# Kernel tuning notes

Hardware: AMD Instinct MI355X
Metric: run time of the kernel (lower is better)

The kernel has to match this reference:

```python
import jax, jax.numpy as jnp
import numpy as np

B, DIN, H, DOUT = 8192, 1024, 2048, 1024
P, E = 4, 6            # n_patches, n_edges
C = H // P             # per-patch feature dim = 512
IDX_I = jnp.array([0, 0, 0, 1, 1, 2])  # i<j pair order matches nested loop
IDX_J = jnp.array([1, 2, 3, 2, 3, 3])


def setup_inputs() -> dict:
    key = jax.random.key(0)
    ks = jax.random.split(key, 12)
    s = 0.02
    return {
        "x": jax.random.normal(ks[0], (B, DIN), jnp.float32),
        "fiber": jax.random.normal(ks[1], (B, C), jnp.float32),  # randn_like(base) in torch fwd
        "W_in": jax.random.normal(ks[2], (DIN, H), jnp.float32) * s,
        "b_in": jnp.zeros((H,), jnp.float32),
        "incidence": jax.random.normal(ks[3], (E, P), jnp.float32) * 0.1,
        "sheaf_maps": jnp.tile((jnp.eye(C, dtype=jnp.float32) * 0.1)[None], (E, 1, 1)),
        "damping": jnp.float32(0.1),
        "Wb": jax.random.normal(ks[4], (P, C, C // 2), jnp.float32) * s,
        "bb": jnp.zeros((P, C // 2), jnp.float32),
        "Wf": jax.random.normal(ks[5], (P, C, C // 2), jnp.float32) * s,
        "bf": jnp.zeros((P, C // 2), jnp.float32),
        "Wt": jax.random.normal(ks[6], (C, C), jnp.float32) * s,
        "bt": jnp.zeros((C,), jnp.float32),
        "Wr": jax.random.normal(ks[7], (E, C, C // 2), jnp.float32) * s,
        "br": jnp.zeros((E, C // 2), jnp.float32),
        "Wg": jax.random.normal(ks[8], (H, H), jnp.float32) * s,
        "bg": jnp.zeros((H,), jnp.float32),
        "Wc": jax.random.normal(ks[9], (H + C, DOUT), jnp.float32) * s,
        "bc": jnp.zeros((DOUT,), jnp.float32),
    }


def reference(x, fiber, W_in, b_in, incidence, sheaf_maps, damping,
              Wb, bb, Wf, bf, Wt, bt, Wr, br, Wg, bg, Wc, bc):
    # input projection + split into P contiguous chunks (stack == reshape)
    h = x @ W_in + b_in                                      # [B, H]
    sections = h.reshape(B, P, C)                            # [B, P, C]

    # --- NeuralSheafLaplacian ---
    # coboundary: incidence-weighted combination of patch sections, then per-edge sheaf map
    weighted = jnp.einsum('ep,bpc->bec', incidence, sections)          # [B, E, C]
    coboundary = jnp.einsum('bec,ecd->bed', weighted, sheaf_maps)      # [B, E, C]
    L = incidence.T @ incidence                                        # [P, P] = delta^T delta
    diffused = sections - damping * jnp.einsum('pq,bqc->bpc', L, sections)
    h1_norm = jnp.linalg.norm(coboundary, axis=-1).mean(axis=-1)       # [B]

    # --- FiberBundleLayer ---
    base = diffused.mean(axis=1)                                       # [B, C]
    b_proj = jnp.einsum('bc,scd->bsd', base, Wb) + bb                  # [B, P, C/2]
    f_proj = jnp.einsum('bc,scd->bsd', fiber, Wf) + bf                 # [B, P, C/2]
    simplices = jnp.concatenate([b_proj, f_proj], axis=-1) @ Wt + bt   # [B, P, C]
    total = simplices.mean(axis=1)                                     # [B, C]

    # --- CohomologyConsistency ---
    si = diffused[:, IDX_I]                                            # [B, E, C]
    sj = diffused[:, IDX_J]                                            # [B, E, C]
    ri = jnp.einsum('bec,ecd->bed', si, Wr) + br
    rj = jnp.einsum('bec,ecd->bed', sj, Wr) + br
    h1_loss = jnp.mean((ri - rj) ** 2, axis=(0, 2)).mean()             # mean of per-pair MSEs
    glued = diffused.reshape(B, H) @ Wg + bg                           # cat(sections) == reshape

    output = jnp.concatenate([glued, total], axis=-1) @ Wc + bc        # [B, DOUT]
    return output, diffused, h1_norm, h1_loss, total
```

## Files before the change

kernel.cpp:

```cpp
#include <hip/hip_runtime.h>
#include <cstdint>

#define B_    8192
#define DIN_  1024
#define H_    2048
#define DOUT_ 1024
#define P4_   4
#define E6_   6
#define C_    512
#define C2_   256

typedef __bf16 bf16x8 __attribute__((ext_vector_type(8)));
typedef float  f32x4  __attribute__((ext_vector_type(4)));

__device__ __forceinline__ unsigned short f2bf_bits(float f) {
    unsigned u = __float_as_uint(f);
    unsigned r = (u + 0x7fffu + ((u >> 16) & 1u)) >> 16;
    return (unsigned short)r;
}
__device__ __forceinline__ float bf2f(unsigned short s) {
    return __uint_as_float(((unsigned)s) << 16);
}

__device__ __forceinline__ void async_load16(void* lds, const void* g) {
    __builtin_amdgcn_global_load_lds(
        (__attribute__((address_space(1))) void*)(uintptr_t)g,
        (__attribute__((address_space(3))) void*)(unsigned int)(uintptr_t)lds,
        16, 0, 0);
}

__global__ void prep_small_k(const float* __restrict__ x, const float* __restrict__ fiber,
                             const float* __restrict__ Wg,
                             const float* __restrict__ Wb, const float* __restrict__ Wf,
                             const float* __restrict__ bb, const float* __restrict__ bfv,
                             const float* __restrict__ Wt, const float* __restrict__ bt,
                             const float* __restrict__ bg, const float* __restrict__ Wc,
                             const float* __restrict__ bc,
                             unsigned short* __restrict__ xb,
                             unsigned short* __restrict__ basefibb,
                             unsigned short* __restrict__ Wgb,
                             unsigned short* __restrict__ WbarCat,
                             float* __restrict__ boutf, float* __restrict__ btotf) {
    int b = blockIdx.x, tid = threadIdx.x;
    if (b < 8192) {
        int i = (b * 256 + tid) * 4;
        float4 v = *(const float4*)(x + i);
        ushort4 o; o.x = f2bf_bits(v.x); o.y = f2bf_bits(v.y);
        o.z = f2bf_bits(v.z); o.w = f2bf_bits(v.w);
        *(ushort4*)(xb + i) = o;
    } else if (b < 12288) {
        int idx4 = ((b - 8192) * 256 + tid) * 4;
        int bb2 = idx4 >> 9, c = idx4 & 511;
        float4 v = *(const float4*)(fiber + idx4);
        ushort4 o; o.x = f2bf_bits(v.x); o.y = f2bf_bits(v.y);
        o.z = f2bf_bits(v.z); o.w = f2bf_bits(v.w);
        *(ushort4*)(basefibb + (long)bb2 * 1024 + 512 + c) = o;
    } else if (b < 16384) {
        int i = ((b - 12288) * 256 + tid) * 4;
        float4 v = *(const float4*)(Wg + i);
        ushort4 o; o.x = f2bf_bits(v.x); o.y = f2bf_bits(v.y);
        o.z = f2bf_bits(v.z); o.w = f2bf_bits(v.w);
        *(ushort4*)(Wgb + i) = o;
    } else if (b < 17408) {
        int z = (b < 16896) ? 0 : 1;
        const float* W = z ? Wf : Wb;
        int id = (b - (z ? 16896 : 16384)) * 256 + tid;
        float s = 0.f;
#pragma unroll
        for (int si = 0; si < 4; si++) s += W[si * (512 * 256) + id];
        WbarCat[z * 131072 + id] = f2bf_bits(0.25f * s);
    } else if (b < 17472) {
        int rel = b - 17408;
        int bx = rel & 3, by = rel >> 2;
        int n = bx * 256 + tid;
        int j0 = by << 7;
        float s = (by == 0) ? bc[n] : 0.f;
#pragma unroll 4
        for (int j = 0; j < 128; j++) s += bg[j0 + j] * Wc[(long)(j0 + j) * 1024 + n];
        atomicAdd(&boutf[n], s);
    } else {
        int n = (b - 17472) * 256 + tid;
        float s = bt[n];
#pragma unroll 4
        for (int d = 0; d < 256; d++) {
            float bbar  = 0.25f * (bb[d]  + bb[256 + d]  + bb[512 + d]  + bb[768 + d]);
            float bfbar = 0.25f * (bfv[d] + bfv[256 + d] + bfv[512 + d] + bfv[768 + d]);
            s += bbar * Wt[d * 512 + n] + bfbar * Wt[(256 + d) * 512 + n];
        }
        btotf[n] = s;
    }
}

__global__ void transpose_all_k(const float* __restrict__ W_in, unsigned short* __restrict__ WinT,
                                const float* __restrict__ Wc,  unsigned short* __restrict__ WcT,
                                unsigned short* __restrict__ WoutT,
                                const float* __restrict__ Wt,  unsigned short* __restrict__ WtT,
                                const float* __restrict__ sheaf, unsigned short* __restrict__ ShT,
                                const float* __restrict__ Wr,  unsigned short* __restrict__ WrT) {
    __shared__ float t[32][33];
    int b = blockIdx.x;
    const float* in; unsigned short* out; unsigned short* out2 = nullptr;
    int R, Cc, gx, rel;
    if (b < 2048)      { rel = b;        in = W_in; out = WinT; R = 1024; Cc = 2048; gx = 64; }
    else if (b < 4608) { rel = b - 2048; in = Wc;   out = WcT;  R = 2560; Cc = 1024; gx = 32; out2 = WoutT; }
    else if (b < 4864) { rel = b - 4608; in = Wt;   out = WtT;  R = 512;  Cc = 512;  gx = 16; }
    else if (b < 6400) { rel = b - 4864; int z = rel >> 8; rel &= 255;
                         in = sheaf + (long)z * 262144; out = ShT + (long)z * 262144;
                         R = 512; Cc = 512; gx = 16; }
    else               { rel = b - 6400; int z = rel >> 7; rel &= 127;
                         in = Wr + (long)z * 131072; out = WrT + (long)z * 131072;
                         R = 512; Cc = 256; gx = 8; }
    int x0 = (rel % gx) << 5, y0 = (rel / gx) << 5;
    int tx = threadIdx.x, ty = threadIdx.y;
#pragma unroll
    for (int j = 0; j < 32; j += 8)
        t[ty + j][tx] = in[(long)(y0 + ty + j) * Cc + x0 + tx];
    __syncthreads();
#pragma unroll
    for (int j = 0; j < 32; j += 8) {
        unsigned short v = f2bf_bits(t[tx][ty + j]);
        long off = (long)(x0 + ty + j) * R + y0 + tx;
        out[off] = v;
        if (out2 && (y0 + tx) >= 2048) out2[off] = v;
    }
}

__global__ void k2_diffuse_k(const unsigned short* __restrict__ hb,
                             const float* __restrict__ incidence,
                             const float* __restrict__ damping,
                             float* __restrict__ outDiff,
                             unsigned short* __restrict__ diffb,
                             unsigned short* __restrict__ basefib,
                             unsigned short* __restrict__ weightedb,
                             unsigned short* __restrict__ debuf) {
    __shared__ float M4[4][4];
    __shared__ float inc2[24];
    int tid = threadIdx.x;
    if (tid < 16) {
        int p = tid >> 2, q = tid & 3;
        float l = 0.f;
#pragma unroll
        for (int e = 0; e < 6; e++) l += incidence[e * 4 + p] * incidence[e * 4 + q];
        M4[p][q] = (p == q ? 1.f : 0.f) - damping[0] * l;
    }
    if (tid < 24) inc2[tid] = incidence[tid];
    __syncthreads();

    int b = blockIdx.x >> 1;
    int c = ((blockIdx.x & 1) << 8) + tid;
    long hoff = (long)b * H_ + c;
    long doff = (long)b * 2560 + c;
    float s0 = bf2f(hb[hoff]);
    float s1 = bf2f(hb[hoff + 512]);
    float s2 = bf2f(hb[hoff + 1024]);
    float s3 = bf2f(hb[hoff + 1536]);

    float d0 = M4[0][0]*s0 + M4[0][1]*s1 + M4[0][2]*s2 + M4[0][3]*s3;
    float d1 = M4[1][0]*s0 + M4[1][1]*s1 + M4[1][2]*s2 + M4[1][3]*s3;
    float d2 = M4[2][0]*s0 + M4[2][1]*s1 + M4[2][2]*s2 + M4[2][3]*s3;
    float d3 = M4[3][0]*s0 + M4[3][1]*s1 + M4[3][2]*s2 + M4[3][3]*s3;

    outDiff[hoff]        = d0;
    outDiff[hoff + 512]  = d1;
    outDiff[hoff + 1024] = d2;
    outDiff[hoff + 1536] = d3;
    diffb[doff]        = f2bf_bits(d0);
    diffb[doff + 512]  = f2bf_bits(d1);
    diffb[doff + 1024] = f2bf_bits(d2);
    diffb[doff + 1536] = f2bf_bits(d3);
    basefib[(long)b * 1024 + c] = f2bf_bits(0.25f * (d0 + d1 + d2 + d3));

#pragma unroll
    for (int e = 0; e < 6; e++) {
        float w = inc2[e*4+0]*s0 + inc2[e*4+1]*s1 + inc2[e*4+2]*s2 + inc2[e*4+3]*s3;
        weightedb[(long)e * (B_ * (long)C_) + (long)b * C_ + c] = f2bf_bits(w);
    }
    float dI[6] = {d0, d0, d0, d1, d1, d2};
    float dJ[6] = {d1, d2, d3, d2, d3, d3};
#pragma unroll
    for (int e = 0; e < 6; e++)
        debuf[(long)e * (B_ * (long)C_) + (long)b * C_ + c] = f2bf_bits(dI[e] - dJ[e]);
}

template <int MODE>
__global__ __launch_bounds__(256, 2)
void gemm_bt_k(const unsigned short* __restrict__ A, long sAz, int lda,
               const unsigned short* __restrict__ Bt, long sBz, int ldb, int K,
               const float* __restrict__ bias,
               unsigned short* __restrict__ Cb, int ldcb,
               float* __restrict__ Cf, int ldcf, long sCz,
               float* __restrict__ red, long sRz) {
    __shared__ __align__(16) unsigned short smA[128 * 64];
    __shared__ __align__(16) unsigned short smB[128 * 64];
    const int tid = threadIdx.x;
    const int lane = tid & 63, w = tid >> 6;
    const int wm = w >> 1, wn = w & 1;
    const int m16 = lane & 15, quad = lane >> 4;
    const int m7 = m16 & 7;

    const int nwg = gridDim.x * gridDim.y;
    const int bid = blockIdx.y * gridDim.x + blockIdx.x;
    const int lid = (nwg & 7) ? bid : (((bid & 7) * (nwg >> 3)) + (bid >> 3));
    const int bx = lid % gridDim.x;
    const int by = lid / gridDim.x;

    A  += (long)blockIdx.z * sAz;
    Bt += (long)blockIdx.z * sBz;
    const long rowA0 = (long)by * 128;
    const long rowB0 = (long)bx * 128;

    f32x4 acc[4][4];
#pragma unroll
    for (int i = 0; i < 4; i++)
#pragma unroll
        for (int j = 0; j < 4; j++) acc[i][j] = f32x4{0.f, 0.f, 0.f, 0.f};

    for (int k0 = 0; k0 < K; k0 += 64) {
#pragma unroll
        for (int i = 0; i < 4; i++) {
            int chunk = i * 256 + tid;
            int row = chunk >> 3;
            int keS = ((chunk & 7) ^ (row & 7)) << 3;
            async_load16(&smA[chunk << 3], A  + (rowA0 + row) * (long)lda + k0 + keS);
            async_load16(&smB[chunk << 3], Bt + (rowB0 + row) * (long)ldb + k0 + keS);
        }
        __syncthreads();
#pragma unroll
        for (int kk = 0; kk < 64; kk += 32) {
            const int pc = (((kk >> 3) + quad) ^ m7) << 3;
            bf16x8 af[4], bfv[4];
#pragma unroll
            for (int i = 0; i < 4; i++) {
                af[i]  = *(const bf16x8*)&smA[((wm << 6) + (i << 4) + m16) * 64 + pc];
                bfv[i] = *(const bf16x8*)&smB[((wn << 6) + (i << 4) + m16) * 64 + pc];
            }
#pragma unroll
            for (int i = 0; i < 4; i++)
#pragma unroll
                for (int j = 0; j < 4; j++)
                    acc[i][j] = __builtin_amdgcn_mfma_f32_16x16x32_bf16(af[i], bfv[j], acc[i][j], 0, 0, 0);
        }
        __syncthreads();
    }

    const long rowBase = rowA0 + (wm << 6);
    const long colBase = rowB0 + (wn << 6);

    if (MODE <= 2) {
        Cb += (long)blockIdx.z * sCz;
        Cf += (long)blockIdx.z * sCz;
#pragma unroll
        for (int j = 0; j < 4; j++) {
            long col = colBase + (j << 4) + m16;
            float bv = bias ? bias[col] : 0.f;
#pragma unroll
            for (int i = 0; i < 4; i++) {
                long row = rowBase + (i << 4) + (quad << 2);
#pragma unroll
                for (int r = 0; r < 4; r++) {
                    float v = acc[i][j][r] + bv;
                    if (MODE == 0 || MODE == 2) Cb[(row + r) * (long)ldcb + col] = f2bf_bits(v);
                    if (MODE == 1 || MODE == 2) Cf[(row + r) * (long)ldcf + col] = v;
                }
            }
        }
    } else if (MODE == 3) {
        float* rz = red + (long)blockIdx.z * sRz;
#pragma unroll
        for (int i = 0; i < 4; i++) {
            float v0 = 0.f, v1 = 0.f, v2 = 0.f, v3 = 0.f;
#pragma unroll
            for (int j = 0; j < 4; j++) {
                float a0 = acc[i][j][0], a1 = acc[i][j][1], a2 = acc[i][j][2], a3 = acc[i][j][3];
                v0 += a0 * a0; v1 += a1 * a1; v2 += a2 * a2; v3 += a3 * a3;
            }
#pragma unroll
            for (int m = 1; m <= 8; m <<= 1) {
                v0 += __shfl_xor(v0, m); v1 += __shfl_xor(v1, m);
                v2 += __shfl_xor(v2, m); v3 += __shfl_xor(v3, m);
            }
            if (m16 == 0) {
                long row = rowBase + (i << 4) + (quad << 2);
                atomicAdd(&rz[row + 0], v0);
                atomicAdd(&rz[row + 1], v1);
                atomicAdd(&rz[row + 2], v2);
                atomicAdd(&rz[row + 3], v3);
            }
        }
    } else {
        float s = 0.f;
#pragma unroll
        for (int i = 0; i < 4; i++)
#pragma unroll
            for (int j = 0; j < 4; j++)
#pragma unroll
                for (int r = 0; r < 4; r++) { float a = acc[i][j][r]; s += a * a; }
#pragma unroll
        for (int m = 1; m <= 32; m <<= 1) s += __shfl_xor(s, m);
        if (lane == 0) atomicAdd(red, s);
    }
}

__device__ __forceinline__ void stage_quarter(unsigned short* ldsT, const unsigned short* g,
                                              long ld, int k0, int isB, int qi, int tid) {
#pragma unroll
    for (int l = 0; l < 2; ++l) {
        int c = l * 512 + tid;
        int i = c >> 3, kc = c & 7;
        int lr = isB ? (((i >> 5) << 6) + (i & 31) + (qi << 5))
                     : (((i >> 6) << 7) + (i & 63) + (qi << 6));
        async_load16(ldsT + lr * 64 + kc * 8,
                     g + (long)lr * ld + k0 + (((kc ^ (lr & 7))) << 3));
    }
}

template <int MODE>
__global__ __launch_bounds__(512, 2)
void gemm256_k(const unsigned short* __restrict__ A, int lda,
               const unsigned short* __restrict__ Bt, int ldb, int K,
               const float* __restrict__ bias,
               unsigned short* __restrict__ Cb, float* __restrict__ Cf, int ldc) {
    extern __shared__ unsigned short sm[];
    unsigned short* smA = sm;
    unsigned short* smB = sm + 2 * 16384;
    const int tid = threadIdx.x;
    const int lane = tid & 63;
    const int wid = tid >> 6;
    const int wm = wid >> 2, wn = wid & 3;
    const int m16 = lane & 15, quad = lane >> 4;
    const int m7 = m16 & 7;

    const int nwg = gridDim.x * gridDim.y;
    const int bid = blockIdx.y * gridDim.x + blockIdx.x;
    const int lid = (nwg & 7) ? bid : (((bid & 7) * (nwg >> 3)) + (bid >> 3));
    const int bx = lid % gridDim.x, by = lid / gridDim.x;
    const long rowA0 = (long)by * 256, rowB0 = (long)bx * 256;

    const unsigned short* gA = A + rowA0 * (long)lda;
    const unsigned short* gB = Bt + rowB0 * (long)ldb;
    const int NT = K >> 6;

    f32x4 acc[8][4];
#pragma unroll
    for (int i = 0; i < 8; i++)
#pragma unroll
        for (int j = 0; j < 4; j++) acc[i][j] = f32x4{0.f, 0.f, 0.f, 0.f};

    stage_quarter(smA,         gA, lda, 0, 0, 0, tid);
    stage_quarter(smB,         gB, ldb, 0, 1, 0, tid);
    stage_quarter(smA,         gA, lda, 0, 0, 1, tid);
    stage_quarter(smB,         gB, ldb, 0, 1, 1, tid);
    if (NT > 1) {
        stage_quarter(smA + 16384, gA, lda, 64, 0, 0, tid);
        stage_quarter(smB + 16384, gB, ldb, 64, 1, 0, tid);
        asm volatile("s_waitcnt vmcnt(4)" ::: "memory");
    } else {
        asm volatile("s_waitcnt vmcnt(0)" ::: "memory");
    }
    __builtin_amdgcn_s_barrier();

    for (int t = 0; t < NT; ++t) {
        const int cur = t & 1;
        unsigned short* cA = smA + cur * 16384;
        unsigned short* cB = smB + cur * 16384;
        unsigned short* nA = smA + (cur ^ 1) * 16384;
        unsigned short* nB = smB + (cur ^ 1) * 16384;
        bf16x8 av[4][2];
#pragma unroll
        for (int q = 0; q < 4; ++q) {
            const int mh = q >> 1, nh = q & 1;
            if (nh == 0) {
#pragma unroll
                for (int fi = 0; fi < 4; ++fi)
#pragma unroll
                    for (int kk = 0; kk < 2; ++kk)
                        av[fi][kk] = *(const bf16x8*)&cA[(wm * 128 + mh * 64 + fi * 16 + m16) * 64
                                                        + ((((kk << 2) + quad)) ^ m7) * 8];
            }
            bf16x8 bv[2][2];
#pragma unroll
            for (int fj = 0; fj < 2; ++fj)
#pragma unroll
                for (int kk = 0; kk < 2; ++kk)
                    bv[fj][kk] = *(const bf16x8*)&cB[(wn * 64 + nh * 32 + fj * 16 + m16) * 64
                                                    + ((((kk << 2) + quad)) ^ m7) * 8];
            if (q == 0) {
                if (t + 1 < NT) stage_quarter(nB, gB, ldb, (t + 1) << 6, 1, 1, tid);
            } else if (q == 1) {
                if (t + 1 < NT) stage_quarter(nA, gA, lda, (t + 1) << 6, 0, 1, tid);
            } else if (q == 2) {
                if (t + 2 < NT) stage_quarter(cA, gA, lda, (t + 2) << 6, 0, 0, tid);
            } else {
                if (t + 2 < NT) stage_quarter(cB, gB, ldb, (t + 2) << 6, 1, 0, tid);
                if (t + 2 < NT)      asm volatile("s_waitcnt vmcnt(4)" ::: "memory");
                else if (t + 1 < NT) asm volatile("s_waitcnt vmcnt(0)" ::: "memory");
            }
            __builtin_amdgcn_s_barrier();
            asm volatile("s_waitcnt lgkmcnt(0)" ::: "memory");
            __builtin_amdgcn_sched_barrier(0);
            __builtin_amdgcn_s_setprio(1);
#pragma unroll
            for (int fi = 0; fi < 4; ++fi)
#pragma unroll
                for (int fj = 0; fj < 2; ++fj)
#pragma unroll
                    for (int kk = 0; kk < 2; ++kk)
                        acc[mh * 4 + fi][nh * 2 + fj] =
                            __builtin_amdgcn_mfma_f32_16x16x32_bf16(av[fi][kk], bv[fj][kk],
                                                                    acc[mh * 4 + fi][nh * 2 + fj], 0, 0, 0);
            __builtin_amdgcn_s_setprio(0);
            __builtin_amdgcn_s_barrier();
        }
    }

#pragma unroll
    for (int fj = 0; fj < 4; ++fj) {
        long col = rowB0 + wn * 64 + fj * 16 + m16;
        float bv2 = bias ? bias[col] : 0.f;
#pragma unroll
        for (int mi = 0; mi < 8; ++mi) {
            long row = rowA0 + wm * 128 + mi * 16 + (quad << 2);
#pragma unroll
            for (int r = 0; r < 4; ++r) {
                float v = acc[mi][fj][r] + bv2;
                if (MODE == 0) Cb[(row + r) * (long)ldc + col] = f2bf_bits(v);
                else           Cf[(row + r) * (long)ldc + col] = v;
            }
        }
    }
}

__global__ void f1_h1norm_k(const float* __restrict__ hn, float* __restrict__ out) {
    int b = blockIdx.x * 256 + threadIdx.x;
    float s = 0.f;
#pragma unroll
    for (int e = 0; e < 6; e++) s += sqrtf(hn[e * B_ + b]);
    out[b] = s * (1.f / 6.f);
}

__global__ void f2_h1loss_k(const float* __restrict__ acc, float* __restrict__ out) {
    if (threadIdx.x == 0) out[0] = acc[0] * (1.f / (8192.f * 6.f * 256.f));
}

extern "C" void kernel_launch(void* const* d_in, const int* in_sizes, int n_in,
                              void* d_out, int out_size, void* d_ws, size_t ws_size,
                              hipStream_t stream) {
    const float* x     = (const float*)d_in[0];
    const float* fiber = (const float*)d_in[1];
    const float* W_in  = (const float*)d_in[2];
    const float* b_in  = (const float*)d_in[3];
    const float* incid = (const float*)d_in[4];
    const float* sheaf = (const float*)d_in[5];
    const float* damp  = (const float*)d_in[6];
    const float* Wb    = (const float*)d_in[7];
    const float* bb    = (const float*)d_in[8];
    const float* Wf    = (const float*)d_in[9];
    const float* bfv   = (const float*)d_in[10];
    const float* Wt    = (const float*)d_in[11];
    const float* bt    = (const float*)d_in[12];
    const float* Wr    = (const float*)d_in[13];
    const float* Wg    = (const float*)d_in[15];
    const float* bg    = (const float*)d_in[16];
    const float* Wc    = (const float*)d_in[17];
    const float* bc    = (const float*)d_in[18];

    float* out      = (float*)d_out;
    float* outDiff  = out + 8388608;
    float* outH1n   = out + 25165824;
    float* outH1l   = out + 25174016;
    float* outTotal = out + 25174017;

    static bool s_attr = false;
    if (!s_attr) {
        (void)hipFuncSetAttribute(reinterpret_cast<const void*>(&gemm256_k<0>),
                                  hipFuncAttributeMaxDynamicSharedMemorySize, 131072);
        (void)hipFuncSetAttribute(reinterpret_cast<const void*>(&gemm256_k<1>),
                                  hipFuncAttributeMaxDynamicSharedMemorySize, 131072);
        s_attr = true;
    }

    char* ws = (char*)d_ws;
    size_t o = 0;
    auto alloc = [&](size_t bytes) { size_t r = o; o += (bytes + 255) & ~(size_t)255; return r; };

    size_t r0 = alloc(50331648);
    unsigned short* xb = (unsigned short*)(ws + r0);
    unsigned short* hb = (unsigned short*)(ws + r0 + 16777216);
    unsigned short* Ab2560    = (unsigned short*)(ws + alloc(41943040));
    unsigned short* basefibb  = (unsigned short*)(ws + alloc(16777216));
    unsigned short* weightedb = (unsigned short*)(ws + alloc(50331648));
    unsigned short* debuf     = (unsigned short*)(ws + alloc(50331648));
    unsigned short* WinT   = (unsigned short*)(ws + alloc(4194304));
    unsigned short* Wgb    = (unsigned short*)(ws + alloc(8388608));
    unsigned short* WcT    = (unsigned short*)(ws + alloc(5242880));
    unsigned short* WoutT  = (unsigned short*)(ws + alloc(5242880));
    unsigned short* WtT    = (unsigned short*)(ws + alloc(524288));
    unsigned short* WrT    = (unsigned short*)(ws + alloc(1572864));
    unsigned short* ShT    = (unsigned short*)(ws + alloc(3145728));
    unsigned short* WbarCat= (unsigned short*)(ws + alloc(524288));
    unsigned short* WcombT = (unsigned short*)(ws + alloc(1048576));
    float* btotf  = (float*)(ws + alloc(2048));
    float* boutf  = (float*)(ws + alloc(4096 + 6 * 8192 * 4 + 256));
    float* hnacc  = boutf + 1024;
    float* lossacc = hnacc + 6 * 8192;

    (void)hipMemsetAsync(boutf, 0, 4096 + 6 * 8192 * 4 + 256, stream);

    prep_small_k<<<17474, 256, 0, stream>>>(x, fiber, Wg, Wb, Wf, bb, bfv, Wt, bt, bg, Wc, bc,
                                            xb, basefibb, Wgb, WbarCat, boutf, btotf);
    transpose_all_k<<<7168, dim3(32, 8), 0, stream>>>(W_in, WinT, Wc, WcT, WoutT,
                                                      Wt, WtT, sheaf, ShT, Wr, WrT);

    gemm_bt_k<0><<<dim3(4, 4, 2), 256, 0, stream>>>(WtT, 256, 512, WbarCat, 131072, 256, 256,
                                                    nullptr, WcombT, 1024, nullptr, 0, 512, nullptr, 0);
    gemm_bt_k<0><<<dim3(16, 8, 1), 256, 0, stream>>>(WcT, 0, 2560, Wgb, 0, 2048, 2048,
                                                     nullptr, WoutT, 2560, nullptr, 0, 0, nullptr, 0);

    gemm256_k<0><<<dim3(8, 32), 512, 131072, stream>>>(xb, DIN_, WinT, DIN_, DIN_,
                                                       b_in, hb, nullptr, H_);
    k2_diffuse_k<<<16384, 256, 0, stream>>>(hb, incid, damp, outDiff, Ab2560, basefibb, weightedb, debuf);

    gemm_bt_k<3><<<dim3(4, 64, 6), 256, 0, stream>>>(weightedb, (long)B_ * C_, C_, ShT, (long)C_ * C_, C_, C_,
                                                     nullptr, nullptr, 0, nullptr, 0, 0, hnacc, B_);
    gemm_bt_k<4><<<dim3(2, 64, 6), 256, 0, stream>>>(debuf, (long)B_ * C_, C_, WrT, (long)C2_ * C_, C_, C_,
                                                     nullptr, nullptr, 0, nullptr, 0, 0, lossacc, 0);
    gemm_bt_k<2><<<dim3(4, 64, 1), 256, 0, stream>>>(basefibb, 0, 1024, WcombT, 0, 1024, 1024,
                                                     btotf, Ab2560 + 2048, 2560, outTotal, C_, 0, nullptr, 0);
    gemm_bt_k<1><<<dim3(8, 64, 1), 256, 0, stream>>>(Ab2560, 0, 2560, WoutT, 0, 2560, 2560,
                                                     boutf, nullptr, 0, out, DOUT_, 0, nullptr, 0);
    f1_h1norm_k<<<32, 256, 0, stream>>>(hnacc, outH1n);
    f2_h1loss_k<<<1, 64, 0, stream>>>(lossacc, outH1l);

    (void)in_sizes; (void)n_in; (void)out_size; (void)ws_size;
}
```

Measured before the change: 584.1 us.

## Merge prep and transpose kernels, vectorize diffuse kernel, merge final reductions

Folds the fp32-to-bf16 conversion kernel and the weight transpose kernel into one launch, with each conversion thread now handling several float4s. The diffuse kernel now processes four channels per thread using ushort4/float4 loads and stores, and the two tiny final kernels become one. The bias-precompute blocks also hoist the averaged biases into shared memory. The aim is fewer launches and wider memory accesses in bandwidth-bound elementwise stages, in exchange for more register pressure and fewer threads per block in the diffuse kernel.

```diff
diff --git a/kernel.cpp b/kernel.cpp
--- a/kernel.cpp
+++ b/kernel.cpp
@@ -21,6 +21,10 @@
 __device__ __forceinline__ float bf2f(unsigned short s) {
     return __uint_as_float(((unsigned)s) << 16);
 }
+__device__ __forceinline__ ushort4 cvt4(float4 v) {
+    ushort4 o; o.x = f2bf_bits(v.x); o.y = f2bf_bits(v.y);
+    o.z = f2bf_bits(v.z); o.w = f2bf_bits(v.w); return o;
+}
 
 __device__ __forceinline__ void async_load16(void* lds, const void* g) {
     __builtin_amdgcn_global_load_lds(
@@ -29,99 +33,98 @@
         16, 0, 0);
 }
 
-__global__ void prep_small_k(const float* __restrict__ x, const float* __restrict__ fiber,
-                             const float* __restrict__ Wg,
-                             const float* __restrict__ Wb, const float* __restrict__ Wf,
-                             const float* __restrict__ bb, const float* __restrict__ bfv,
-                             const float* __restrict__ Wt, const float* __restrict__ bt,
-                             const float* __restrict__ bg, const float* __restrict__ Wc,
-                             const float* __restrict__ bc,
-                             unsigned short* __restrict__ xb,
-                             unsigned short* __restrict__ basefibb,
-                             unsigned short* __restrict__ Wgb,
-                             unsigned short* __restrict__ WbarCat,
-                             float* __restrict__ boutf, float* __restrict__ btotf) {
+__global__ void prep_all_k(const float* __restrict__ x, const float* __restrict__ fiber,
+                           const float* __restrict__ Wg,
+                           const float* __restrict__ Wb, const float* __restrict__ Wf,
+                           const float* __restrict__ bb, const float* __restrict__ bfv,
+                           const float* __restrict__ Wt, const float* __restrict__ bt,
+                           const float* __restrict__ bg, const float* __restrict__ Wc,
+                           const float* __restrict__ bc,
+                           const float* __restrict__ W_in,
+                           const float* __restrict__ sheaf, const float* __restrict__ Wr,
+                           unsigned short* __restrict__ xb,
+                           unsigned short* __restrict__ basefibb,
+                           unsigned short* __restrict__ Wgb,
+                           unsigned short* __restrict__ WbarCat,
+                           float* __restrict__ boutf, float* __restrict__ btotf,
+                           unsigned short* __restrict__ WinT, unsigned short* __restrict__ WcT,
+                           unsigned short* __restrict__ WoutT, unsigned short* __restrict__ WtT,
+                           unsigned short* __restrict__ ShT,  unsigned short* __restrict__ WrT) {
+    __shared__ float smf[1056];
     int b = blockIdx.x, tid = threadIdx.x;
-    if (b < 8192) {
-        int i = (b * 256 + tid) * 4;
-        float4 v = *(const float4*)(x + i);
-        ushort4 o; o.x = f2bf_bits(v.x); o.y = f2bf_bits(v.y);
-        o.z = f2bf_bits(v.z); o.w = f2bf_bits(v.w);
-        *(ushort4*)(xb + i) = o;
-    } else if (b < 12288) {
-        int idx4 = ((b - 8192) * 256 + tid) * 4;
-        int bb2 = idx4 >> 9, c = idx4 & 511;
-        float4 v = *(const float4*)(fiber + idx4);
-        ushort4 o; o.x = f2bf_bits(v.x); o.y = f2bf_bits(v.y);
-        o.z = f2bf_bits(v.z); o.w = f2bf_bits(v.w);
-        *(ushort4*)(basefibb + (long)bb2 * 1024 + 512 + c) = o;
-    } else if (b < 16384) {
-        int i = ((b - 12288) * 256 + tid) * 4;
-        float4 v = *(const float4*)(Wg + i);
-        ushort4 o; o.x = f2bf_bits(v.x); o.y = f2bf_bits(v.y);
-        o.z = f2bf_bits(v.z); o.w = f2bf_bits(v.w);
-        *(ushort4*)(Wgb + i) = o;
-    } else if (b < 17408) {
-        int z = (b < 16896) ? 0 : 1;
+    if (b < 2048) {
+        int base = b * 256 + tid;
+        float4 v0 = *(const float4*)(x + (long)base * 4);
+        float4 v1 = *(const float4*)(x + (long)(base +  524288) * 4);
+        float4 v2 = *(const float4*)(x + (long)(base + 1048576) * 4);
+        float4 v3 = *(const float4*)(x + (long)(base + 1572864) * 4);
+        float4 v4 = *(const float4*)(fiber + (long)base * 4);
+        float4 v5 = *(const float4*)(fiber + (long)(base + 524288) * 4);
+        float4 v6 = *(const float4*)(Wg + (long)base * 4);
+        float4 v7 = *(const float4*)(Wg + (long)(base + 524288) * 4);
+        *(ushort4*)(xb + (long)base * 4)                  = cvt4(v0);
+        *(ushort4*)(xb + (long)(base +  524288) * 4)      = cvt4(v1);
+        *(ushort4*)(xb + (long)(base + 1048576) * 4)      = cvt4(v2);
+        *(ushort4*)(xb + (long)(base + 1572864) * 4)      = cvt4(v3);
+        {   int idx4 = base * 4;          int b2 = idx4 >> 9, c = idx4 & 511;
+            *(ushort4*)(basefibb + (long)b2 * 1024 + 512 + c) = cvt4(v4); }
+        {   int idx4 = (base + 524288) * 4; int b2 = idx4 >> 9, c = idx4 & 511;
+            *(ushort4*)(basefibb + (long)b2 * 1024 + 512 + c) = cvt4(v5); }
+        *(ushort4*)(Wgb + (long)base * 4)                 = cvt4(v6);
+        *(ushort4*)(Wgb + (long)(base + 524288) * 4)      = cvt4(v7);
+    } else if (b < 3072) {
+        int z = (b < 2560) ? 0 : 1;
         const float* W = z ? Wf : Wb;
-        int id = (b - (z ? 16896 : 16384)) * 256 + tid;
+        int id = (b - (z ? 2560 : 2048)) * 256 + tid;
         float s = 0.f;
 #pragma unroll
         for (int si = 0; si < 4; si++) s += W[si * (512 * 256) + id];
         WbarCat[z * 131072 + id] = f2bf_bits(0.25f * s);
-    } else if (b < 17472) {
-        int rel = b - 17408;
+    } else if (b < 3200) {
+        int rel = b - 3072;
         int bx = rel & 3, by = rel >> 2;
         int n = bx * 256 + tid;
-        int j0 = by << 7;
+        int j0 = by << 6;
         float s = (by == 0) ? bc[n] : 0.f;
-#pragma unroll 4
-        for (int j = 0; j < 128; j++) s += bg[j0 + j] * Wc[(long)(j0 + j) * 1024 + n];
+#pragma unroll 8
+        for (int j = 0; j < 64; j++) s += bg[j0 + j] * Wc[(long)(j0 + j) * 1024 + n];
         atomicAdd(&boutf[n], s);
+    } else if (b < 3202) {
+        smf[tid]       = 0.25f * (bb[tid]  + bb[256 + tid]  + bb[512 + tid]  + bb[768 + tid]);
+        smf[256 + tid] = 0.25f * (bfv[tid] + bfv[256 + tid] + bfv[512 + tid] + bfv[768 + tid]);
+        __syncthreads();
+        int n = (b - 3200) * 256 + tid;
+        float s = bt[n];
+#pragma unroll 8
+        for (int d = 0; d < 256; d++)
+            s += smf[d] * Wt[d * 512 + n] + smf[256 + d] * Wt[(256 + d) * 512 + n];
+        btotf[n] = s;
     } else {
-        int n = (b - 17472) * 256 + tid;
-        float s = bt[n];
-#pragma unroll 4
-        for (int d = 0; d < 256; d++) {
-            float bbar  = 0.25f * (bb[d]  + bb[256 + d]  + bb[512 + d]  + bb[768 + d]);
-            float bfbar = 0.25f * (bfv[d] + bfv[256 + d] + bfv[512 + d] + bfv[768 + d]);
-            s += bbar * Wt[d * 512 + n] + bfbar * Wt[(256 + d) * 512 + n];
-        }
-        btotf[n] = s;
-    }
-}
-
-__global__ void transpose_all_k(const float* __restrict__ W_in, unsigned short* __restrict__ WinT,
-                                const float* __restrict__ Wc,  unsigned short* __restrict__ WcT,
-                                unsigned short* __restrict__ WoutT,
-                                const float* __restrict__ Wt,  unsigned short* __restrict__ WtT,
-                                const float* __restrict__ sheaf, unsigned short* __restrict__ ShT,
-                                const float* __restrict__ Wr,  unsigned short* __restrict__ WrT) {
-    __shared__ float t[32][33];
-    int b = blockIdx.x;
-    const float* in; unsigned short* out; unsigned short* out2 = nullptr;
-    int R, Cc, gx, rel;
-    if (b < 2048)      { rel = b;        in = W_in; out = WinT; R = 1024; Cc = 2048; gx = 64; }
-    else if (b < 4608) { rel = b - 2048; in = Wc;   out = WcT;  R = 2560; Cc = 1024; gx = 32; out2 = WoutT; }
-    else if (b < 4864) { rel = b - 4608; in = Wt;   out = WtT;  R = 512;  Cc = 512;  gx = 16; }
-    else if (b < 6400) { rel = b - 4864; int z = rel >> 8; rel &= 255;
-                         in = sheaf + (long)z * 262144; out = ShT + (long)z * 262144;
-                         R = 512; Cc = 512; gx = 16; }
-    else               { rel = b - 6400; int z = rel >> 7; rel &= 127;
-                         in = Wr + (long)z * 131072; out = WrT + (long)z * 131072;
-                         R = 512; Cc = 256; gx = 8; }
-    int x0 = (rel % gx) << 5, y0 = (rel / gx) << 5;
-    int tx = threadIdx.x, ty = threadIdx.y;
-#pragma unroll
-    for (int j = 0; j < 32; j += 8)
-        t[ty + j][tx] = in[(long)(y0 + ty + j) * Cc + x0 + tx];
-    __syncthreads();
-#pragma unroll
-    for (int j = 0; j < 32; j += 8) {
-        unsigned short v = f2bf_bits(t[tx][ty + j]);
-        long off = (long)(x0 + ty + j) * R + y0 + tx;
-        out[off] = v;
-        if (out2 && (y0 + tx) >= 2048) out2[off] = v;
+        int rel = b - 3202;
+        const float* in; unsigned short* out; unsigned short* out2 = nullptr;
+        int R, Cc, gx;
+        if (rel < 2048)      {               in = W_in; out = WinT; R = 1024; Cc = 2048; gx = 64; }
+        else if (rel < 4608) { rel -= 2048;  in = Wc;   out = WcT;  R = 2560; Cc = 1024; gx = 32; out2 = WoutT; }
+        else if (rel < 4864) { rel -= 4608;  in = Wt;   out = WtT;  R = 512;  Cc = 512;  gx = 16; }
+        else if (rel < 6400) { rel -= 4864;  int z = rel >> 8; rel &= 255;
+                               in = sheaf + (long)z * 262144; out = ShT + (long)z * 262144;
+                               R = 512; Cc = 512; gx = 16; }
+        else                 { rel -= 6400;  int z = rel >> 7; rel &= 127;
+                               in = Wr + (long)z * 131072; out = WrT + (long)z * 131072;
+                               R = 512; Cc = 256; gx = 8; }
+        int x0 = (rel % gx) << 5, y0 = (rel / gx) << 5;
+        int tx = tid & 31, ty = tid >> 5;
+#pragma unroll
+        for (int j = 0; j < 32; j += 8)
+            smf[(ty + j) * 33 + tx] = in[(long)(y0 + ty + j) * Cc + x0 + tx];
+        __syncthreads();
+#pragma unroll
+        for (int j = 0; j < 32; j += 8) {
+            unsigned short v = f2bf_bits(smf[tx * 33 + ty + j]);
+            long off = (long)(x0 + ty + j) * R + y0 + tx;
+            out[off] = v;
+            if (out2 && (y0 + tx) >= 2048) out2[off] = v;
+        }
     }
 }
 
@@ -133,7 +136,7 @@
                              unsigned short* __restrict__ basefib,
                              unsigned short* __restrict__ weightedb,
                              unsigned short* __restrict__ debuf) {
-    __shared__ float M4[4][4];
+    __shared__ float M4[16];
     __shared__ float inc2[24];
     int tid = threadIdx.x;
     if (tid < 16) {
@@ -141,45 +144,63 @@
         float l = 0.f;
 #pragma unroll
         for (int e = 0; e < 6; e++) l += incidence[e * 4 + p] * incidence[e * 4 + q];
-        M4[p][q] = (p == q ? 1.f : 0.f) - damping[0] * l;
+        M4[tid] = (p == q ? 1.f : 0.f) - damping[0] * l;
     }
     if (tid < 24) inc2[tid] = incidence[tid];
     __syncthreads();
 
-    int b = blockIdx.x >> 1;
-    int c = ((blockIdx.x & 1) << 8) + tid;
-    long hoff = (long)b * H_ + c;
-    long doff = (long)b * 2560 + c;
-    float s0 = bf2f(hb[hoff]);
-    float s1 = bf2f(hb[hoff + 512]);
-    float s2 = bf2f(hb[hoff + 1024]);
-    float s3 = bf2f(hb[hoff + 1536]);
-
-    float d0 = M4[0][0]*s0 + M4[0][1]*s1 + M4[0][2]*s2 + M4[0][3]*s3;
-    float d1 = M4[1][0]*s0 + M4[1][1]*s1 + M4[1][2]*s2 + M4[1][3]*s3;
-    float d2 = M4[2][0]*s0 + M4[2][1]*s1 + M4[2][2]*s2 + M4[2][3]*s3;
-    float d3 = M4[3][0]*s0 + M4[3][1]*s1 + M4[3][2]*s2 + M4[3][3]*s3;
-
-    outDiff[hoff]        = d0;
-    outDiff[hoff + 512]  = d1;
-    outDiff[hoff + 1024] = d2;
-    outDiff[hoff + 1536] = d3;
-    diffb[doff]        = f2bf_bits(d0);
-    diffb[doff + 512]  = f2bf_bits(d1);
-    diffb[doff + 1024] = f2bf_bits(d2);
-    diffb[doff + 1536] = f2bf_bits(d3);
-    basefib[(long)b * 1024 + c] = f2bf_bits(0.25f * (d0 + d1 + d2 + d3));
-
+    int b = blockIdx.x;
+    int c0 = tid << 2;
+    long hoff = (long)b * H_ + c0;
+    long doff = (long)b * 2560 + c0;
+    ushort4 u0 = *(const ushort4*)(hb + hoff);
+    ushort4 u1 = *(const ushort4*)(hb + hoff + 512);
+    ushort4 u2 = *(const ushort4*)(hb + hoff + 1024);
+    ushort4 u3 = *(const ushort4*)(hb + hoff + 1536);
+    const unsigned short* p0 = (const unsigned short*)&u0;
+    const unsigned short* p1 = (const unsigned short*)&u1;
+    const unsigned short* p2 = (const unsigned short*)&u2;
+    const unsigned short* p3 = (const unsigned short*)&u3;
+
+    float d[4][4], w[6][4], de[6][4], bs[4];
+#pragma unroll
+    for (int j = 0; j < 4; ++j) {
+        float s0 = bf2f(p0[j]), s1 = bf2f(p1[j]), s2 = bf2f(p2[j]), s3 = bf2f(p3[j]);
+        d[0][j] = M4[0]*s0  + M4[1]*s1  + M4[2]*s2  + M4[3]*s3;
+        d[1][j] = M4[4]*s0  + M4[5]*s1  + M4[6]*s2  + M4[7]*s3;
+        d[2][j] = M4[8]*s0  + M4[9]*s1  + M4[10]*s2 + M4[11]*s3;
+        d[3][j] = M4[12]*s0 + M4[13]*s1 + M4[14]*s2 + M4[15]*s3;
+        bs[j] = 0.25f * (d[0][j] + d[1][j] + d[2][j] + d[3][j]);
+#pragma unroll
+        for (int e = 0; e < 6; e++)
+            w[e][j] = inc2[e*4+0]*s0 + inc2[e*4+1]*s1 + inc2[e*4+2]*s2 + inc2[e*4+3]*s3;
+        de[0][j] = d[0][j] - d[1][j];
+        de[1][j] = d[0][j] - d[2][j];
+        de[2][j] = d[0][j] - d[3][j];
+        de[3][j] = d[1][j] - d[2][j];
+        de[4][j] = d[1][j] - d[3][j];
+        de[5][j] = d[2][j] - d[3][j];
+    }
+#pragma unroll
+    for (int r = 0; r < 4; ++r) {
+        *(float4*)(outDiff + hoff + r * 512) = float4{d[r][0], d[r][1], d[r][2], d[r][3]};
+        ushort4 t; t.x = f2bf_bits(d[r][0]); t.y = f2bf_bits(d[r][1]);
+        t.z = f2bf_bits(d[r][2]); t.w = f2bf_bits(d[r][3]);
+        *(ushort4*)(diffb + doff + r * 512) = t;
+    }
+    {   ushort4 t; t.x = f2bf_bits(bs[0]); t.y = f2bf_bits(bs[1]);
+        t.z = f2bf_bits(bs[2]); t.w = f2bf_bits(bs[3]);
+        *(ushort4*)(basefib + (long)b * 1024 + c0) = t; }
 #pragma unroll
     for (int e = 0; e < 6; e++) {
-        float w = inc2[e*4+0]*s0 + inc2[e*4+1]*s1 + inc2[e*4+2]*s2 + inc2[e*4+3]*s3;
-        weightedb[(long)e * (B_ * (long)C_) + (long)b * C_ + c] = f2bf_bits(w);
-    }
-    float dI[6] = {d0, d0, d0, d1, d1, d2};
-    float dJ[6] = {d1, d2, d3, d2, d3, d3};
-#pragma unroll
-    for (int e = 0; e < 6; e++)
-        debuf[(long)e * (B_ * (long)C_) + (long)b * C_ + c] = f2bf_bits(dI[e] - dJ[e]);
+        long eoff = (long)e * (B_ * (long)C_) + (long)b * C_ + c0;
+        ushort4 tw; tw.x = f2bf_bits(w[e][0]); tw.y = f2bf_bits(w[e][1]);
+        tw.z = f2bf_bits(w[e][2]); tw.w = f2bf_bits(w[e][3]);
+        *(ushort4*)(weightedb + eoff) = tw;
+        ushort4 td; td.x = f2bf_bits(de[e][0]); td.y = f2bf_bits(de[e][1]);
+        td.z = f2bf_bits(de[e][2]); td.w = f2bf_bits(de[e][3]);
+        *(ushort4*)(debuf + eoff) = td;
+    }
 }
 
 template <int MODE>
@@ -430,16 +451,17 @@
     }
 }
 
-__global__ void f1_h1norm_k(const float* __restrict__ hn, float* __restrict__ out) {
-    int b = blockIdx.x * 256 + threadIdx.x;
-    float s = 0.f;
-#pragma unroll
-    for (int e = 0; e < 6; e++) s += sqrtf(hn[e * B_ + b]);
-    out[b] = s * (1.f / 6.f);
-}
-
-__global__ void f2_h1loss_k(const float* __restrict__ acc, float* __restrict__ out) {
-    if (threadIdx.x == 0) out[0] = acc[0] * (1.f / (8192.f * 6.f * 256.f));
+__global__ void finals_k(const float* __restrict__ hn, float* __restrict__ outN,
+                         const float* __restrict__ acc, float* __restrict__ outL) {
+    if (blockIdx.x < 32) {
+        int b = blockIdx.x * 256 + threadIdx.x;
+        float s = 0.f;
+#pragma unroll
+        for (int e = 0; e < 6; e++) s += sqrtf(hn[e * B_ + b]);
+        outN[b] = s * (1.f / 6.f);
+    } else if (threadIdx.x == 0) {
+        outL[0] = acc[0] * (1.f / (8192.f * 6.f * 256.f));
+    }
 }
 
 extern "C" void kernel_launch(void* const* d_in, const int* in_sizes, int n_in,
@@ -506,10 +528,10 @@
 
     (void)hipMemsetAsync(boutf, 0, 4096 + 6 * 8192 * 4 + 256, stream);
 
-    prep_small_k<<<17474, 256, 0, stream>>>(x, fiber, Wg, Wb, Wf, bb, bfv, Wt, bt, bg, Wc, bc,
-                                            xb, basefibb, Wgb, WbarCat, boutf, btotf);
-    transpose_all_k<<<7168, dim3(32, 8), 0, stream>>>(W_in, WinT, Wc, WcT, WoutT,
-                                                      Wt, WtT, sheaf, ShT, Wr, WrT);
+    prep_all_k<<<10370, 256, 0, stream>>>(x, fiber, Wg, Wb, Wf, bb, bfv, Wt, bt, bg, Wc, bc,
+                                          W_in, sheaf, Wr,
+                                          xb, basefibb, Wgb, WbarCat, boutf, btotf,
+                                          WinT, WcT, WoutT, WtT, ShT, WrT);
 
     gemm_bt_k<0><<<dim3(4, 4, 2), 256, 0, stream>>>(WtT, 256, 512, WbarCat, 131072, 256, 256,
                                                     nullptr, WcombT, 1024, nullptr, 0, 512, nullptr, 0);
@@ -518,7 +540,7 @@
 
     gemm256_k<0><<<dim3(8, 32), 512, 131072, stream>>>(xb, DIN_, WinT, DIN_, DIN_,
                                                        b_in, hb, nullptr, H_);
-    k2_diffuse_k<<<16384, 256, 0, stream>>>(hb, incid, damp, outDiff, Ab2560, basefibb, weightedb, debuf);
+    k2_diffuse_k<<<8192, 128, 0, stream>>>(hb, incid, damp, outDiff, Ab2560, basefibb, weightedb, debuf);
 
     gemm_bt_k<3><<<dim3(4, 64, 6), 256, 0, stream>>>(weightedb, (long)B_ * C_, C_, ShT, (long)C_ * C_, C_, C_,
                                                      nullptr, nullptr, 0, nullptr, 0, 0, hnacc, B_);
@@ -528,8 +550,7 @@
                                                      btotf, Ab2560 + 2048, 2560, outTotal, C_, 0, nullptr, 0);
     gemm_bt_k<1><<<dim3(8, 64, 1), 256, 0, stream>>>(Ab2560, 0, 2560, WoutT, 0, 2560, 2560,
                                                      boutf, nullptr, 0, out, DOUT_, 0, nullptr, 0);
-    f1_h1norm_k<<<32, 256, 0, stream>>>(hnacc, outH1n);
-    f2_h1loss_k<<<1, 64, 0, stream>>>(lossacc, outH1l);
+    finals_k<<<33, 256, 0, stream>>>(hnacc, outH1n, lossacc, outH1l);
 
     (void)in_sizes; (void)n_in; (void)out_size; (void)ws_size;
 }
```

New measurement: 554.7 us. 5.0% less time.
